# Kernel optimization log

Measured on AMD Instinct MI355X. Metric: run time of the kernel, lower is better.

The kernel has to match this reference:

```python
import jax, jax.numpy as jnp
import numpy as np

N = 50000       # nodes
E = 1600000     # edges
G = 16          # graphs in batch
NUMCHIP = 16    # node features
NUMEDGE = 8     # edge features
H = 32          # hidden_channels
NEG = 0.2       # LeakyReLU slope (PyG GAT default)


def _wegat_conv(x, ea, src, dst, Wn, bn, We, be, att):
    """Edge-weighted GAT conv: returns (node_out [N,H], edge_out [E,NUMEDGE])."""
    xn = x @ Wn + bn                      # [N, H]
    ea2 = ea @ We + be                    # [E, NUMEDGE]
    xi = xn[dst]                          # [E, H] target features
    xj = xn[src]                          # [E, H] source features
    logits = jnp.concatenate([xi, xj, ea2], axis=-1) @ att   # [E]
    logits = jax.nn.leaky_relu(logits, NEG)
    # numerically stable softmax over incoming edges per destination node
    m = jax.ops.segment_max(logits, dst, num_segments=N)
    m = jnp.where(jnp.isfinite(m), m, 0.0)
    p = jnp.exp(logits - m[dst])
    s = jax.ops.segment_sum(p, dst, num_segments=N)
    alpha = p / (s[dst] + 1e-16)          # [E]
    out = jax.ops.segment_sum(xj * alpha[:, None], dst, num_segments=N)  # [N, H]
    return out, ea2


def setup_inputs() -> dict:
    key = jax.random.key(0)
    ks = jax.random.split(key, 24)

    def gl(k, shape):
        fan_in = shape[0] if len(shape) > 1 else shape[0]
        return jax.random.normal(k, shape, dtype=jnp.float32) * (1.0 / np.sqrt(fan_in))

    inp = {
        'x': jax.random.normal(ks[0], (N, NUMCHIP), dtype=jnp.float32),
        'edge_attr': jax.random.normal(ks[1], (E, NUMEDGE), dtype=jnp.float32),
        'edge_index': jax.random.randint(ks[2], (2, E), 0, N, dtype=jnp.int64),
        'batch': jnp.sort(jax.random.randint(ks[3], (N,), 0, G, dtype=jnp.int64)),
        # layer 1
        'Wn1': gl(ks[4], (NUMCHIP, H)), 'bn1': jnp.zeros((H,), jnp.float32),
        'We1': gl(ks[5], (NUMEDGE, NUMEDGE)), 'be1': jnp.zeros((NUMEDGE,), jnp.float32),
        'att1': gl(ks[6], (2 * H + NUMEDGE,)),
        # layer 2
        'Wn2': gl(ks[7], (H, H)), 'bn2': jnp.zeros((H,), jnp.float32),
        'We2': gl(ks[8], (NUMEDGE, NUMEDGE)), 'be2': jnp.zeros((NUMEDGE,), jnp.float32),
        'att2': gl(ks[9], (2 * H + NUMEDGE,)),
        # layer 3
        'Wn3': gl(ks[10], (H, H)), 'bn3': jnp.zeros((H,), jnp.float32),
        'We3': gl(ks[11], (NUMEDGE, NUMEDGE)), 'be3': jnp.zeros((NUMEDGE,), jnp.float32),
        'att3': gl(ks[12], (2 * H + NUMEDGE,)),
        # head
        'Wlin': gl(ks[13], (H, 1)), 'blin': jnp.zeros((1,), jnp.float32),
    }
    return inp


def reference(x, edge_attr, edge_index, batch,
              Wn1, bn1, We1, be1, att1,
              Wn2, bn2, We2, be2, att2,
              Wn3, bn3, We3, be3, att3,
              Wlin, blin):
    src, dst = edge_index[0], edge_index[1]
    x1, ea1 = _wegat_conv(x, edge_attr, src, dst, Wn1, bn1, We1, be1, att1)
    x1 = jax.nn.relu(x1)  # NOTE: original's edge_attr.relu() is a discarded no-op
    x2, ea2 = _wegat_conv(x1, ea1, src, dst, Wn2, bn2, We2, be2, att2)
    x2 = jax.nn.relu(x2)
    x3, _ = _wegat_conv(x2, ea2, src, dst, Wn3, bn3, We3, be3, att3)
    # global mean pool over graphs
    sums = jax.ops.segment_sum(x3, batch, num_segments=G)                   # [G, H]
    cnts = jax.ops.segment_sum(jnp.ones((N,), x3.dtype), batch, num_segments=G)
    pooled = sums / jnp.maximum(cnts, 1.0)[:, None]
    return pooled @ Wlin + blin  # [G, 1]
```

## Files before the change

kernel.cpp:

```cpp
#include <hip/hip_runtime.h>
#include <math.h>


__global__ __launch_bounds__(256) void zero_kernel(int* cnt, float* pool, int n, int npool) {
    int i = blockIdx.x * blockDim.x + threadIdx.x;
    if (i < n) cnt[i] = 0;
    if (i < npool) pool[i] = 0.f;
}

__global__ __launch_bounds__(256) void hist_kernel(const int* __restrict__ dst, int* cnt, int E) {
    int e = blockIdx.x * blockDim.x + threadIdx.x;
    if (e < E) atomicAdd(&cnt[dst[e]], 1);
}

__global__ __launch_bounds__(1024) void scan_kernel(const int* __restrict__ cnt,
                                                    int* rowptr, int* cursor, int n) {
    __shared__ int sums[1024];
    int t = threadIdx.x;
    int CH = (n + 1023) >> 10;
    int s0 = t * CH;
    int s1 = min(n, s0 + CH);
    int local = 0;
    for (int i = s0; i < s1; i++) local += cnt[i];
    sums[t] = local;
    __syncthreads();
    for (int off = 1; off < 1024; off <<= 1) {
        int v = (t >= off) ? sums[t - off] : 0;
        __syncthreads();
        sums[t] += v;
        __syncthreads();
    }
    int run = (t == 0) ? 0 : sums[t - 1];
    for (int i = s0; i < s1; i++) {
        rowptr[i] = run;
        cursor[i] = run;
        run += cnt[i];
    }
    if (t == 1023) rowptr[n] = sums[1023];
}

__global__ __launch_bounds__(256) void scatter_kernel(const int* __restrict__ src,
                                                      const int* __restrict__ dst,
                                                      int* cursor, int* eid, int* esrc, int E) {
    int e = blockIdx.x * blockDim.x + threadIdx.x;
    if (e >= E) return;
    int d = dst[e];
    int pos = atomicAdd(&cursor[d], 1);
    eid[pos] = e;
    esrc[pos] = src[e];
}

template <int IN>
__global__ __launch_bounds__(256) void node_linear(const float* __restrict__ xin,
                                                   const float* __restrict__ Wn,
                                                   const float* __restrict__ bn,
                                                   const float* __restrict__ att,
                                                   float* __restrict__ xn,
                                                   float* __restrict__ ai,
                                                   float* __restrict__ aj, int n) {
    int t = blockIdx.x * blockDim.x + threadIdx.x;
    int node = t >> 5;
    int h = t & 31;
    if (node >= n) return;
    float acc = bn[h];
#pragma unroll
    for (int k = 0; k < IN; k++) {
        acc = fmaf(xin[node * IN + k], Wn[k * 32 + h], acc);
    }
    xn[node * 32 + h] = acc;
    float pi = acc * att[h];
    float pj = acc * att[32 + h];
#pragma unroll
    for (int off = 16; off > 0; off >>= 1) {
        pi += __shfl_xor(pi, off);
        pj += __shfl_xor(pj, off);
    }
    if (h == 0) {
        ai[node] = pi;
        aj[node] = pj;
    }
}

__global__ __launch_bounds__(256) void edge_linear(const float* ein,
                                                   const float* __restrict__ We,
                                                   const float* __restrict__ be,
                                                   const float* __restrict__ atte,
                                                   float* eout, float* __restrict__ ae,
                                                   int E, int store) {
    int e = blockIdx.x * blockDim.x + threadIdx.x;
    if (e >= E) return;
    const float4* p = (const float4*)(ein + (size_t)e * 8);
    float4 x0 = p[0], x1 = p[1];
    float in[8] = {x0.x, x0.y, x0.z, x0.w, x1.x, x1.y, x1.z, x1.w};
    float o[8];
    float dot = 0.f;
#pragma unroll
    for (int j = 0; j < 8; j++) {
        float a = be[j];
#pragma unroll
        for (int k = 0; k < 8; k++) a = fmaf(in[k], We[k * 8 + j], a);
        o[j] = a;
        dot = fmaf(a, atte[j], dot);
    }
    ae[e] = dot;
    if (store) {
        float4* q = (float4*)(eout + (size_t)e * 8);
        q[0] = make_float4(o[0], o[1], o[2], o[3]);
        q[1] = make_float4(o[4], o[5], o[6], o[7]);
    }
}

__global__ __launch_bounds__(256) void gat_aggregate(const float* __restrict__ xn,
                                                     const float* __restrict__ ai,
                                                     const float* __restrict__ aj,
                                                     const float* __restrict__ ae,
                                                     const int* __restrict__ rowptr,
                                                     const int* __restrict__ eid,
                                                     const int* __restrict__ esrc,
                                                     float* __restrict__ xout,
                                                     int n, int relu_out) {
    int wave = (blockIdx.x * blockDim.x + threadIdx.x) >> 6;
    int lane = threadIdx.x & 63;
    if (wave >= n) return;
    int node = wave;
    int row = rowptr[node];
    int deg = rowptr[node + 1] - row;
    int h = lane & 31;
    if (deg == 0) {
        if (lane < 32) xout[node * 32 + h] = 0.f;
        return;
    }
    float a_i = ai[node];

    float mx = -INFINITY;
    for (int k = lane; k < deg; k += 64) {
        float lg = a_i + aj[esrc[row + k]] + ae[eid[row + k]];
        lg = (lg >= 0.f) ? lg : 0.2f * lg;
        mx = fmaxf(mx, lg);
    }
#pragma unroll
    for (int off = 32; off > 0; off >>= 1) mx = fmaxf(mx, __shfl_xor(mx, off));

    float acc = 0.f, psum = 0.f;
    int half = lane >> 5;
    for (int base = 0; base < deg; base += 64) {
        int k = base + lane;
        float p = 0.f;
        int s = 0;
        if (k < deg) {
            int e = eid[row + k];
            s = esrc[row + k];
            float lg = a_i + aj[s] + ae[e];
            lg = (lg >= 0.f) ? lg : 0.2f * lg;
            p = expf(lg - mx);
        }
        psum += p;
        int csize = min(64, deg - base);
        for (int j = half; j < csize; j += 2) {
            float pj = __shfl(p, j);
            int sj = __shfl(s, j);
            acc = fmaf(pj, xn[sj * 32 + h], acc);
        }
    }
#pragma unroll
    for (int off = 32; off > 0; off >>= 1) psum += __shfl_xor(psum, off);
    acc += __shfl_xor(acc, 32);

    float o = acc / (psum + 1e-16f);
    if (relu_out) o = fmaxf(o, 0.f);
    if (lane < 32) xout[node * 32 + h] = o;
}

__global__ __launch_bounds__(256) void pool_kernel(const float* __restrict__ x3,
                                                   const int* __restrict__ batch,
                                                   float* pool, int n) {
    int h = threadIdx.x & 31;
    int rowl = threadIdx.x >> 5;
    int per = (n + gridDim.x - 1) / gridDim.x;
    int n0 = blockIdx.x * per;
    int n1 = min(n, n0 + per);
    float acc = 0.f;
    int curg = -1;
    for (int i = n0 + rowl; i < n1; i += 8) {
        int g = batch[i];
        if (g != curg) {
            if (curg >= 0) atomicAdd(&pool[curg * 32 + h], acc);
            acc = 0.f;
            curg = g;
        }
        acc += x3[i * 32 + h];
    }
    if (curg >= 0) atomicAdd(&pool[curg * 32 + h], acc);
}

__global__ __launch_bounds__(64) void head_kernel(const float* __restrict__ pool,
                                                  const int* __restrict__ batch,
                                                  const float* __restrict__ Wlin,
                                                  const float* __restrict__ blin,
                                                  float* out, int n, int G) {
    int g = threadIdx.x;
    if (g >= G) return;
    float s = 0.f;
#pragma unroll
    for (int k = 0; k < 32; k++) s = fmaf(pool[g * 32 + k], Wlin[k], s);
    int lo = 0, hi = n;
    while (lo < hi) {
        int m = (lo + hi) >> 1;
        if (batch[m] < g) lo = m + 1; else hi = m;
    }
    int start = lo;
    lo = 0; hi = n;
    while (lo < hi) {
        int m = (lo + hi) >> 1;
        if (batch[m] < g + 1) lo = m + 1; else hi = m;
    }
    float c = fmaxf((float)(lo - start), 1.f);
    out[g] = s / c + blin[0];
}

extern "C" void kernel_launch(void* const* d_in, const int* in_sizes, int n_in,
                              void* d_out, int out_size, void* d_ws, size_t ws_size,
                              hipStream_t stream) {
    const float* x    = (const float*)d_in[0];
    const float* ea0  = (const float*)d_in[1];
    const int* ei     = (const int*)d_in[2];
    const int* batch  = (const int*)d_in[3];
    const float* Wn[3] = {(const float*)d_in[4], (const float*)d_in[9],  (const float*)d_in[14]};
    const float* bn[3] = {(const float*)d_in[5], (const float*)d_in[10], (const float*)d_in[15]};
    const float* We[3] = {(const float*)d_in[6], (const float*)d_in[11], (const float*)d_in[16]};
    const float* be[3] = {(const float*)d_in[7], (const float*)d_in[12], (const float*)d_in[17]};
    const float* att[3]= {(const float*)d_in[8], (const float*)d_in[13], (const float*)d_in[18]};
    const float* Wlin = (const float*)d_in[19];
    const float* blin = (const float*)d_in[20];
    float* out = (float*)d_out;

    const int N = in_sizes[0] / 16;
    const int E = in_sizes[1] / 8;
    const int G = out_size;
    (void)n_in; (void)ws_size;

    const int* srcp = ei;
    const int* dstp = ei + E;

    char* base = (char*)d_ws;
    size_t off = 0;
    auto carve = [&](size_t bytes) -> void* {
        void* p = base + off;
        off = (off + bytes + 255) & ~(size_t)255;
        return p;
    };
    float* xnA   = (float*)carve((size_t)N * 32 * 4);
    float* xnB   = (float*)carve((size_t)N * 32 * 4);
    float* ai    = (float*)carve((size_t)N * 4);
    float* aj    = (float*)carve((size_t)N * 4);
    float* ea    = (float*)carve((size_t)E * 8 * 4);
    float* ae    = (float*)carve((size_t)E * 4);
    int* cnt     = (int*)carve((size_t)N * 4);
    int* rowptr  = (int*)carve((size_t)(N + 1) * 4);
    int* cursor  = (int*)carve((size_t)N * 4);
    int* eid     = (int*)carve((size_t)E * 4);
    int* esrc    = (int*)carve((size_t)E * 4);
    float* pool  = (float*)carve((size_t)G * 32 * 4);

    int ebks = (E + 255) / 256;
    int nhbks = (N * 32 + 255) / 256;
    int aggbks = (N + 3) / 4;

    zero_kernel<<<(N + 255) / 256, 256, 0, stream>>>(cnt, pool, N, G * 32);
    hist_kernel<<<ebks, 256, 0, stream>>>(dstp, cnt, E);
    scan_kernel<<<1, 1024, 0, stream>>>(cnt, rowptr, cursor, N);
    scatter_kernel<<<ebks, 256, 0, stream>>>(srcp, dstp, cursor, eid, esrc, E);

    node_linear<16><<<nhbks, 256, 0, stream>>>(x, Wn[0], bn[0], att[0], xnA, ai, aj, N);
    edge_linear<<<ebks, 256, 0, stream>>>(ea0, We[0], be[0], att[0] + 64, ea, ae, E, 1);
    gat_aggregate<<<aggbks, 256, 0, stream>>>(xnA, ai, aj, ae, rowptr, eid, esrc, xnB, N, 1);

    node_linear<32><<<nhbks, 256, 0, stream>>>(xnB, Wn[1], bn[1], att[1], xnA, ai, aj, N);
    edge_linear<<<ebks, 256, 0, stream>>>(ea, We[1], be[1], att[1] + 64, ea, ae, E, 1);
    gat_aggregate<<<aggbks, 256, 0, stream>>>(xnA, ai, aj, ae, rowptr, eid, esrc, xnB, N, 1);

    node_linear<32><<<nhbks, 256, 0, stream>>>(xnB, Wn[2], bn[2], att[2], xnA, ai, aj, N);
    edge_linear<<<ebks, 256, 0, stream>>>(ea, We[2], be[2], att[2] + 64, nullptr, ae, E, 0);
    gat_aggregate<<<aggbks, 256, 0, stream>>>(xnA, ai, aj, ae, rowptr, eid, esrc, xnB, N, 0);

    pool_kernel<<<128, 256, 0, stream>>>(xnB, batch, pool, N);
    head_kernel<<<1, 64, 0, stream>>>(pool, batch, Wlin, blin, out, N, G);
}
```

Measured before the change: 778.7 us.

## Fuse three edge linear layers into one kernel and pack CSR src/eid

The edge-feature chain across the three layers does not depend on node features, so the three edge_linear launches are fused into one edge_chain kernel. It keeps intermediate edge features in registers and writes only the three per-edge attention scalars, which removes the E*8 float writes and re-reads of edge attributes. The CSR source and edge-id arrays are interleaved into one int2 array so the aggregate kernel issues one 8-byte load per edge instead of two. The zero kernel is replaced with hipMemsetAsync calls, in exchange for two extra E-sized scratch buffers for ae2 and ae3.

Measured after the change: 741.4 us. 1.05x faster.

```diff
diff --git a/kernel.cpp b/kernel.cpp
--- a/kernel.cpp
+++ b/kernel.cpp
@@ -1,12 +1,6 @@
 #include <hip/hip_runtime.h>
 #include <math.h>
 
-
-__global__ __launch_bounds__(256) void zero_kernel(int* cnt, float* pool, int n, int npool) {
-    int i = blockIdx.x * blockDim.x + threadIdx.x;
-    if (i < n) cnt[i] = 0;
-    if (i < npool) pool[i] = 0.f;
-}
 
 __global__ __launch_bounds__(256) void hist_kernel(const int* __restrict__ dst, int* cnt, int E) {
     int e = blockIdx.x * blockDim.x + threadIdx.x;
@@ -41,13 +35,12 @@
 
 __global__ __launch_bounds__(256) void scatter_kernel(const int* __restrict__ src,
                                                       const int* __restrict__ dst,
-                                                      int* cursor, int* eid, int* esrc, int E) {
+                                                      int* cursor, int2* __restrict__ pack, int E) {
     int e = blockIdx.x * blockDim.x + threadIdx.x;
     if (e >= E) return;
     int d = dst[e];
     int pos = atomicAdd(&cursor[d], 1);
-    eid[pos] = e;
-    esrc[pos] = src[e];
+    pack[pos] = make_int2(src[e], e);
 }
 
 template <int IN>
@@ -81,33 +74,45 @@
     }
 }
 
-__global__ __launch_bounds__(256) void edge_linear(const float* ein,
-                                                   const float* __restrict__ We,
-                                                   const float* __restrict__ be,
-                                                   const float* __restrict__ atte,
-                                                   float* eout, float* __restrict__ ae,
-                                                   int E, int store) {
+__global__ __launch_bounds__(256) void edge_chain(
+    const float* __restrict__ ein,
+    const float* __restrict__ We1, const float* __restrict__ be1, const float* __restrict__ a1,
+    const float* __restrict__ We2, const float* __restrict__ be2, const float* __restrict__ a2,
+    const float* __restrict__ We3, const float* __restrict__ be3, const float* __restrict__ a3,
+    float* __restrict__ ae1, float* __restrict__ ae2, float* __restrict__ ae3, int E) {
     int e = blockIdx.x * blockDim.x + threadIdx.x;
     if (e >= E) return;
     const float4* p = (const float4*)(ein + (size_t)e * 8);
     float4 x0 = p[0], x1 = p[1];
-    float in[8] = {x0.x, x0.y, x0.z, x0.w, x1.x, x1.y, x1.z, x1.w};
-    float o[8];
-    float dot = 0.f;
+    float v[8] = {x0.x, x0.y, x0.z, x0.w, x1.x, x1.y, x1.z, x1.w};
+    float t[8], u[8];
+    float d1 = 0.f, d2 = 0.f, d3 = 0.f;
 #pragma unroll
     for (int j = 0; j < 8; j++) {
-        float a = be[j];
-#pragma unroll
-        for (int k = 0; k < 8; k++) a = fmaf(in[k], We[k * 8 + j], a);
-        o[j] = a;
-        dot = fmaf(a, atte[j], dot);
-    }
-    ae[e] = dot;
-    if (store) {
-        float4* q = (float4*)(eout + (size_t)e * 8);
-        q[0] = make_float4(o[0], o[1], o[2], o[3]);
-        q[1] = make_float4(o[4], o[5], o[6], o[7]);
-    }
+        float a = be1[j];
+#pragma unroll
+        for (int k = 0; k < 8; k++) a = fmaf(v[k], We1[k * 8 + j], a);
+        t[j] = a;
+        d1 = fmaf(a, a1[j], d1);
+    }
+#pragma unroll
+    for (int j = 0; j < 8; j++) {
+        float a = be2[j];
+#pragma unroll
+        for (int k = 0; k < 8; k++) a = fmaf(t[k], We2[k * 8 + j], a);
+        u[j] = a;
+        d2 = fmaf(a, a2[j], d2);
+    }
+#pragma unroll
+    for (int j = 0; j < 8; j++) {
+        float a = be3[j];
+#pragma unroll
+        for (int k = 0; k < 8; k++) a = fmaf(u[k], We3[k * 8 + j], a);
+        d3 = fmaf(a, a3[j], d3);
+    }
+    ae1[e] = d1;
+    ae2[e] = d2;
+    ae3[e] = d3;
 }
 
 __global__ __launch_bounds__(256) void gat_aggregate(const float* __restrict__ xn,
@@ -115,8 +120,7 @@
                                                      const float* __restrict__ aj,
                                                      const float* __restrict__ ae,
                                                      const int* __restrict__ rowptr,
-                                                     const int* __restrict__ eid,
-                                                     const int* __restrict__ esrc,
+                                                     const int2* __restrict__ pack,
                                                      float* __restrict__ xout,
                                                      int n, int relu_out) {
     int wave = (blockIdx.x * blockDim.x + threadIdx.x) >> 6;
@@ -131,10 +135,12 @@
         return;
     }
     float a_i = ai[node];
+    const int2* pk = pack + row;
 
     float mx = -INFINITY;
     for (int k = lane; k < deg; k += 64) {
-        float lg = a_i + aj[esrc[row + k]] + ae[eid[row + k]];
+        int2 q = pk[k];
+        float lg = a_i + aj[q.x] + ae[q.y];
         lg = (lg >= 0.f) ? lg : 0.2f * lg;
         mx = fmaxf(mx, lg);
     }
@@ -148,9 +154,9 @@
         float p = 0.f;
         int s = 0;
         if (k < deg) {
-            int e = eid[row + k];
-            s = esrc[row + k];
-            float lg = a_i + aj[s] + ae[e];
+            int2 q = pk[k];
+            s = q.x;
+            float lg = a_i + aj[s] + ae[q.y];
             lg = (lg >= 0.f) ? lg : 0.2f * lg;
             p = expf(lg - mx);
         }
@@ -253,35 +259,39 @@
     float* xnB   = (float*)carve((size_t)N * 32 * 4);
     float* ai    = (float*)carve((size_t)N * 4);
     float* aj    = (float*)carve((size_t)N * 4);
-    float* ea    = (float*)carve((size_t)E * 8 * 4);
-    float* ae    = (float*)carve((size_t)E * 4);
+    float* ae1   = (float*)carve((size_t)E * 4);
+    float* ae2   = (float*)carve((size_t)E * 4);
+    float* ae3   = (float*)carve((size_t)E * 4);
     int* cnt     = (int*)carve((size_t)N * 4);
     int* rowptr  = (int*)carve((size_t)(N + 1) * 4);
     int* cursor  = (int*)carve((size_t)N * 4);
-    int* eid     = (int*)carve((size_t)E * 4);
-    int* esrc    = (int*)carve((size_t)E * 4);
+    int2* pack   = (int2*)carve((size_t)E * 8);
     float* pool  = (float*)carve((size_t)G * 32 * 4);
 
     int ebks = (E + 255) / 256;
     int nhbks = (N * 32 + 255) / 256;
     int aggbks = (N + 3) / 4;
 
-    zero_kernel<<<(N + 255) / 256, 256, 0, stream>>>(cnt, pool, N, G * 32);
+    hipMemsetAsync(cnt, 0, (size_t)N * 4, stream);
+    hipMemsetAsync(pool, 0, (size_t)G * 32 * 4, stream);
     hist_kernel<<<ebks, 256, 0, stream>>>(dstp, cnt, E);
     scan_kernel<<<1, 1024, 0, stream>>>(cnt, rowptr, cursor, N);
-    scatter_kernel<<<ebks, 256, 0, stream>>>(srcp, dstp, cursor, eid, esrc, E);
+    scatter_kernel<<<ebks, 256, 0, stream>>>(srcp, dstp, cursor, pack, E);
+
+    edge_chain<<<ebks, 256, 0, stream>>>(ea0,
+                                         We[0], be[0], att[0] + 64,
+                                         We[1], be[1], att[1] + 64,
+                                         We[2], be[2], att[2] + 64,
+                                         ae1, ae2, ae3, E);
 
     node_linear<16><<<nhbks, 256, 0, stream>>>(x, Wn[0], bn[0], att[0], xnA, ai, aj, N);
-    edge_linear<<<ebks, 256, 0, stream>>>(ea0, We[0], be[0], att[0] + 64, ea, ae, E, 1);
-    gat_aggregate<<<aggbks, 256, 0, stream>>>(xnA, ai, aj, ae, rowptr, eid, esrc, xnB, N, 1);
+    gat_aggregate<<<aggbks, 256, 0, stream>>>(xnA, ai, aj, ae1, rowptr, pack, xnB, N, 1);
 
     node_linear<32><<<nhbks, 256, 0, stream>>>(xnB, Wn[1], bn[1], att[1], xnA, ai, aj, N);
-    edge_linear<<<ebks, 256, 0, stream>>>(ea, We[1], be[1], att[1] + 64, ea, ae, E, 1);
-    gat_aggregate<<<aggbks, 256, 0, stream>>>(xnA, ai, aj, ae, rowptr, eid, esrc, xnB, N, 1);
+    gat_aggregate<<<aggbks, 256, 0, stream>>>(xnA, ai, aj, ae2, rowptr, pack, xnB, N, 1);
 
     node_linear<32><<<nhbks, 256, 0, stream>>>(xnB, Wn[2], bn[2], att[2], xnA, ai, aj, N);
-    edge_linear<<<ebks, 256, 0, stream>>>(ea, We[2], be[2], att[2] + 64, nullptr, ae, E, 0);
-    gat_aggregate<<<aggbks, 256, 0, stream>>>(xnA, ai, aj, ae, rowptr, eid, esrc, xnB, N, 0);
+    gat_aggregate<<<aggbks, 256, 0, stream>>>(xnA, ai, aj, ae3, rowptr, pack, xnB, N, 0);
 
     pool_kernel<<<128, 256, 0, stream>>>(xnB, batch, pool, N);
     head_kernel<<<1, 64, 0, stream>>>(pool, batch, Wlin, blin, out, N, G);
```
